# Kernel tuning notes

Hardware: AMD Instinct MI355X
Metric: run time of the kernel (lower is better)

The kernel has to match this reference:

```python
import jax, jax.numpy as jnp
import numpy as np
from jax import lax

WIN = 9
PAD = WIN // 2  # floor(9/2) = 4, 'same' spatial output


def _box_sum(x):
    # 3D sliding-window sum via conv with a ones kernel [1,1,9,9,9]
    k = jnp.ones((1, 1, WIN, WIN, WIN), x.dtype)
    return lax.conv_general_dilated(
        x, k,
        window_strides=(1, 1, 1),
        padding=[(PAD, PAD)] * 3,
        dimension_numbers=('NCDHW', 'OIDHW', 'NCDHW'),
    )


def setup_inputs() -> dict:
    key = jax.random.key(0)
    k1, k2 = jax.random.split(key)
    shape = (2, 1, 160, 160, 160)  # [B, C=1, D, H, W] 3D volumes
    return {
        'y_true': jax.random.normal(k1, shape, dtype=jnp.float32),
        'y_pred': jax.random.normal(k2, shape, dtype=jnp.float32),
    }


def reference(y_true, y_pred):
    win_size = float(WIN ** 3)  # 729
    I, J = y_true, y_pred
    I_sum = _box_sum(I)
    J_sum = _box_sum(J)
    I2_sum = _box_sum(I * I)
    J2_sum = _box_sum(J * J)
    IJ_sum = _box_sum(I * J)
    u_I = I_sum / win_size
    u_J = J_sum / win_size
    cross = IJ_sum - u_J * I_sum - u_I * J_sum + u_I * u_J * win_size
    I_var = I2_sum - 2.0 * u_I * I_sum + u_I * u_I * win_size
    J_var = J2_sum - 2.0 * u_J * J_sum + u_J * u_J * win_size
    cc = cross * cross / (I_var * J_var + 1e-5)
    return -jnp.mean(cc)
```

## Files before the change

kernel.cpp:

```cpp
#include <hip/hip_runtime.h>


#define NB   2
#define NDIM 160
#define TILE 32
#define RE   40
#define HS   42
#define DCHUNK 32
#define NDCHUNK (NDIM / DCHUNK)
#define NSLICE (DCHUNK + 8)
#define NBLK ((NDIM/TILE)*(NDIM/TILE)*NB*NDCHUNK)
#define NTHR 1024
#define SLICE_SZ (NDIM * NDIM)

__device__ __forceinline__ float both_halves_sum(float a) {
#if __has_builtin(__builtin_amdgcn_permlane32_swap)
    typedef int v2i __attribute__((ext_vector_type(2)));
    v2i r = __builtin_amdgcn_permlane32_swap(__float_as_int(a),
                                             __float_as_int(a), false, false);
    return __int_as_float(r[0]) + __int_as_float(r[1]);
#else
    return a + __shfl_xor(a, 32, 64);
#endif
}

__global__ __launch_bounds__(NTHR)
void ncc_main(const float* __restrict__ I, const float* __restrict__ J,
              double* __restrict__ out_acc, unsigned int* __restrict__ out_cnt,
              float* __restrict__ out) {
    const int t  = threadIdx.x;
    const int tx = t & 31;
    const int ty = t >> 5;
    const int half = ty & 1;
    const int w0 = blockIdx.x * TILE;
    const int h0 = blockIdx.y * TILE;
    const int b  = blockIdx.z / NDCHUNK;
    const int d0 = (blockIdx.z % NDCHUNK) * DCHUNK;

    const float* Ib = I + (size_t)b * NDIM * SLICE_SZ;
    const float* Jb = J + (size_t)b * NDIM * SLICE_SZ;

    __shared__ alignas(16) float sI[2][RE][HS];
    __shared__ alignas(16) float sJ[2][RE][HS];
    __shared__ float4 rs4[RE][TILE + 1];
    __shared__ float  rss[RE][TILE + 1];
    __shared__ double wsum[NTHR / 64];

    const int e1 = t + NTHR;
    const int r0 = t / RE,  c0 = t - r0 * RE;
    const int r1 = e1 / RE, c1 = e1 - r1 * RE;
    const int h_0 = h0 - 4 + r0, w_0 = w0 - 4 + c0;
    const int h_1 = h0 - 4 + r1, w_1 = w0 - 4 + c1;
    const bool has1 = (e1 < RE * RE);
    const bool in0 = ((unsigned)h_0 < NDIM) && ((unsigned)w_0 < NDIM);
    const bool in1 = has1 && ((unsigned)h_1 < NDIM) && ((unsigned)w_1 < NDIM);
    const int idx0 = h_0 * NDIM + w_0;
    const int idx1 = h_1 * NDIM + w_1;

    const int br  = t >> 4;
    const int bw0 = (t & 15) * 2;
    const int rb = (ty & ~1) + half * 5;
    const int re = (ty & ~1) + (half ? 0 : 9);

    float ring[9][5];
#pragma unroll
    for (int k = 0; k < 9; ++k)
#pragma unroll
        for (int c = 0; c < 5; ++c) ring[k][c] = 0.0f;

    float acc[5] = {0.f, 0.f, 0.f, 0.f, 0.f};
    double csum = 0.0;
    const float inv_win = 1.0f / 729.0f;
    int cur = 0;

    {
        const int dz0 = d0 - 4;
        if ((unsigned)dz0 < NDIM) {
            const float* Iz = Ib + (size_t)dz0 * SLICE_SZ;
            const float* Jz = Jb + (size_t)dz0 * SLICE_SZ;
            sI[0][r0][c0] = in0 ? Iz[idx0] : 0.f;
            sJ[0][r0][c0] = in0 ? Jz[idx0] : 0.f;
            if (has1) {
                sI[0][r1][c1] = in1 ? Iz[idx1] : 0.f;
                sJ[0][r1][c1] = in1 ? Jz[idx1] : 0.f;
            }
        }
        __syncthreads();
    }

    for (int o = 0; o < 5; ++o) {
#pragma unroll
        for (int j = 0; j < 9; ++j) {
            const int step = o * 9 + j;
            const int dz = d0 - 4 + step;
            float s[5] = {0.f, 0.f, 0.f, 0.f, 0.f};
            if (step < NSLICE) {
                const int dzn = dz + 1;
                const bool pf = (step + 1 < NSLICE) && ((unsigned)dzn < NDIM);
                float pvi0 = 0.f, pvj0 = 0.f, pvi1 = 0.f, pvj1 = 0.f;
                if (pf) {
                    const float* Iz = Ib + (size_t)dzn * SLICE_SZ;
                    const float* Jz = Jb + (size_t)dzn * SLICE_SZ;
                    if (in0) { pvi0 = Iz[idx0]; pvj0 = Jz[idx0]; }
                    if (in1) { pvi1 = Iz[idx1]; pvj1 = Jz[idx1]; }
                }
                if ((unsigned)dz < NDIM && t < 640) {
                    const float2* pI = (const float2*)(&sI[cur][br][bw0]);
                    const float2* pJ = (const float2*)(&sJ[cur][br][bw0]);
                    float2 iA = pI[0], iB = pI[1], iC = pI[2], iD = pI[3], iE = pI[4];
                    float2 jA = pJ[0], jB = pJ[1], jC = pJ[2], jD = pJ[3], jE = pJ[4];
                    float aI  = iA.x + iA.y + iB.x + iB.y + iC.x + iC.y
                              + iD.x + iD.y + iE.x;
                    float aJ  = jA.x + jA.y + jB.x + jB.y + jC.x + jC.y
                              + jD.x + jD.y + jE.x;
                    float aI2 = iA.x*iA.x + iA.y*iA.y + iB.x*iB.x + iB.y*iB.y
                              + iC.x*iC.x + iC.y*iC.y + iD.x*iD.x + iD.y*iD.y
                              + iE.x*iE.x;
                    float aJ2 = jA.x*jA.x + jA.y*jA.y + jB.x*jB.x + jB.y*jB.y
                              + jC.x*jC.x + jC.y*jC.y + jD.x*jD.x + jD.y*jD.y
                              + jE.x*jE.x;
                    float aIJ = iA.x*jA.x + iA.y*jA.y + iB.x*jB.x + iB.y*jB.y
                              + iC.x*jC.x + iC.y*jC.y + iD.x*jD.x + iD.y*jD.y
                              + iE.x*jE.x;
                    rs4[br][bw0] = make_float4(aI, aJ, aI2, aJ2);
                    rss[br][bw0] = aIJ;
                    aI  += iE.y - iA.x;
                    aJ  += jE.y - jA.x;
                    aI2 += iE.y*iE.y - iA.x*iA.x;
                    aJ2 += jE.y*jE.y - jA.x*jA.x;
                    aIJ += iE.y*jE.y - iA.x*jA.x;
                    rs4[br][bw0 + 1] = make_float4(aI, aJ, aI2, aJ2);
                    rss[br][bw0 + 1] = aIJ;
                }
                if (pf) {
                    const int nxt = cur ^ 1;
                    sI[nxt][r0][c0] = pvi0;
                    sJ[nxt][r0][c0] = pvj0;
                    if (has1) { sI[nxt][r1][c1] = pvi1; sJ[nxt][r1][c1] = pvj1; }
                }
                __syncthreads();
                if ((unsigned)dz < NDIM) {
                    float a0 = 0.f, a1 = 0.f, a2 = 0.f, a3 = 0.f, a4 = 0.f;
#pragma unroll
                    for (int k = 0; k < 5; ++k) {
                        float4 v = rs4[rb + k][tx];
                        a0 += v.x; a1 += v.y; a2 += v.z; a3 += v.w;
                        a4 += rss[rb + k][tx];
                    }
                    float4 ev = rs4[re][tx];
                    float  es = rss[re][tx];
                    s[0] = both_halves_sum(a0) - ev.x;
                    s[1] = both_halves_sum(a1) - ev.y;
                    s[2] = both_halves_sum(a2) - ev.z;
                    s[3] = both_halves_sum(a3) - ev.w;
                    s[4] = both_halves_sum(a4) - es;
                }
                __syncthreads();
                cur ^= 1;
            }
#pragma unroll
            for (int c = 0; c < 5; ++c) {
                acc[c] += s[c] - ring[j][c];
                ring[j][c] = s[c];
            }
            if (step >= 8 && step < 8 + DCHUNK) {
                float Is = acc[0], Js = acc[1];
                float I2 = acc[2], J2 = acc[3], IJ = acc[4];
                float cross = IJ - Is * Js * inv_win;
                float Ivar  = I2 - Is * Is * inv_win;
                float Jvar  = J2 - Js * Js * inv_win;
                float cc = cross * cross / (Ivar * Jvar + 1e-5f);
                csum += (double)cc;
            }
        }
    }

#pragma unroll
    for (int off = 32; off > 0; off >>= 1)
        csum += __shfl_down(csum, off, 64);
    if ((t & 63) == 0) wsum[t >> 6] = csum;
    __syncthreads();
    if (t == 0) {
        double total = 0.0;
#pragma unroll
        for (int wv = 0; wv < NTHR / 64; ++wv) total += wsum[wv];
        atomicAdd(out_acc, total);
        __threadfence();
        unsigned int old = atomicAdd(out_cnt, 1u);
        if (old == NBLK - 1) {
            double fin = atomicAdd(out_acc, 0.0);
            out[0] = (float)(-fin / 8192000.0);
        }
    }
}

extern "C" void kernel_launch(void* const* d_in, const int* in_sizes, int n_in,
                              void* d_out, int out_size, void* d_ws, size_t ws_size,
                              hipStream_t stream) {
    const float* I = (const float*)d_in[0];
    const float* J = (const float*)d_in[1];
    double* acc = (double*)d_ws;
    unsigned int* cnt = (unsigned int*)((char*)d_ws + 8);

    hipMemsetAsync(d_ws, 0, 16, stream);

    dim3 grid(NDIM / TILE, NDIM / TILE, NB * NDCHUNK);
    ncc_main<<<grid, NTHR, 0, stream>>>(I, J, acc, cnt, (float*)d_out);
}
```

Measured before the change: 140.2 us.

## Load halo slices as float4 and double-buffer row sums to drop a barrier

Slice staging now uses 128-bit float4 global loads. Each of 960 threads loads four contiguous floats of either I or J into a 48-wide padded row, replacing four scalar loads per thread. The row-sum buffers rs4/rss are double-buffered by slice parity, so the second __syncthreads per slice is removed. This halves the barriers per step and cuts load instruction count, at the cost of more shared memory. Correctness relies on the 4-aligned tile edges, where a float4 is either fully inside the volume or fully outside.

```diff
diff --git a/kernel.cpp b/kernel.cpp
--- a/kernel.cpp
+++ b/kernel.cpp
@@ -5,7 +5,7 @@
 #define NDIM 160
 #define TILE 32
 #define RE   40
-#define HS   42
+#define F4W  12
 #define DCHUNK 32
 #define NDCHUNK (NDIM / DCHUNK)
 #define NSLICE (DCHUNK + 8)
@@ -40,22 +40,20 @@
     const float* Ib = I + (size_t)b * NDIM * SLICE_SZ;
     const float* Jb = J + (size_t)b * NDIM * SLICE_SZ;
 
-    __shared__ alignas(16) float sI[2][RE][HS];
-    __shared__ alignas(16) float sJ[2][RE][HS];
-    __shared__ float4 rs4[RE][TILE + 1];
-    __shared__ float  rss[RE][TILE + 1];
+    __shared__ float4 sH[2][2][RE][F4W];
+    __shared__ float4 rs4[2][RE][TILE + 1];
+    __shared__ float  rss[2][RE][TILE + 1];
     __shared__ double wsum[NTHR / 64];
 
-    const int e1 = t + NTHR;
-    const int r0 = t / RE,  c0 = t - r0 * RE;
-    const int r1 = e1 / RE, c1 = e1 - r1 * RE;
-    const int h_0 = h0 - 4 + r0, w_0 = w0 - 4 + c0;
-    const int h_1 = h0 - 4 + r1, w_1 = w0 - 4 + c1;
-    const bool has1 = (e1 < RE * RE);
-    const bool in0 = ((unsigned)h_0 < NDIM) && ((unsigned)w_0 < NDIM);
-    const bool in1 = has1 && ((unsigned)h_1 < NDIM) && ((unsigned)w_1 < NDIM);
-    const int idx0 = h_0 * NDIM + w_0;
-    const int idx1 = h_1 * NDIM + w_1;
+    const int sa   = (t / 480) & 1;
+    const int item = t - (t / 480) * 480;
+    const int sr   = item / F4W;
+    const int sf   = item - sr * F4W;
+    const int sgr  = h0 - 4 + sr;
+    const int sgc  = w0 - 8 + 4 * sf;
+    const bool sval = (t < 960) && ((unsigned)sgr < NDIM) &&
+                      ((unsigned)sgc < NDIM) && (sgc + 3 < NDIM);
+    const int sgoff = sgr * NDIM + sgc;
 
     const int br  = t >> 4;
     const int bw0 = (t & 15) * 2;
@@ -71,19 +69,15 @@
     float acc[5] = {0.f, 0.f, 0.f, 0.f, 0.f};
     double csum = 0.0;
     const float inv_win = 1.0f / 729.0f;
-    int cur = 0;
+    int bi = 0;
 
     {
         const int dz0 = d0 - 4;
-        if ((unsigned)dz0 < NDIM) {
-            const float* Iz = Ib + (size_t)dz0 * SLICE_SZ;
-            const float* Jz = Jb + (size_t)dz0 * SLICE_SZ;
-            sI[0][r0][c0] = in0 ? Iz[idx0] : 0.f;
-            sJ[0][r0][c0] = in0 ? Jz[idx0] : 0.f;
-            if (has1) {
-                sI[0][r1][c1] = in1 ? Iz[idx1] : 0.f;
-                sJ[0][r1][c1] = in1 ? Jz[idx1] : 0.f;
-            }
+        if ((unsigned)dz0 < NDIM && t < 960) {
+            const float* base = (sa ? Jb : Ib) + (size_t)dz0 * SLICE_SZ;
+            float4 v = make_float4(0.f, 0.f, 0.f, 0.f);
+            if (sval) v = *reinterpret_cast<const float4*>(base + sgoff);
+            sH[0][sa][sr][sf] = v;
         }
         __syncthreads();
     }
@@ -97,16 +91,16 @@
             if (step < NSLICE) {
                 const int dzn = dz + 1;
                 const bool pf = (step + 1 < NSLICE) && ((unsigned)dzn < NDIM);
-                float pvi0 = 0.f, pvj0 = 0.f, pvi1 = 0.f, pvj1 = 0.f;
-                if (pf) {
-                    const float* Iz = Ib + (size_t)dzn * SLICE_SZ;
-                    const float* Jz = Jb + (size_t)dzn * SLICE_SZ;
-                    if (in0) { pvi0 = Iz[idx0]; pvj0 = Jz[idx0]; }
-                    if (in1) { pvi1 = Iz[idx1]; pvj1 = Jz[idx1]; }
+                float4 pv = make_float4(0.f, 0.f, 0.f, 0.f);
+                if (pf && sval) {
+                    const float* base = (sa ? Jb : Ib) + (size_t)dzn * SLICE_SZ;
+                    pv = *reinterpret_cast<const float4*>(base + sgoff);
                 }
                 if ((unsigned)dz < NDIM && t < 640) {
-                    const float2* pI = (const float2*)(&sI[cur][br][bw0]);
-                    const float2* pJ = (const float2*)(&sJ[cur][br][bw0]);
+                    const float* rowI = (const float*)sH[bi][0][br];
+                    const float* rowJ = (const float*)sH[bi][1][br];
+                    const float2* pI = (const float2*)(rowI + bw0 + 4);
+                    const float2* pJ = (const float2*)(rowJ + bw0 + 4);
                     float2 iA = pI[0], iB = pI[1], iC = pI[2], iD = pI[3], iE = pI[4];
                     float2 jA = pJ[0], jB = pJ[1], jC = pJ[2], jD = pJ[3], jE = pJ[4];
                     float aI  = iA.x + iA.y + iB.x + iB.y + iC.x + iC.y
@@ -122,41 +116,35 @@
                     float aIJ = iA.x*jA.x + iA.y*jA.y + iB.x*jB.x + iB.y*jB.y
                               + iC.x*jC.x + iC.y*jC.y + iD.x*jD.x + iD.y*jD.y
                               + iE.x*jE.x;
-                    rs4[br][bw0] = make_float4(aI, aJ, aI2, aJ2);
-                    rss[br][bw0] = aIJ;
+                    rs4[bi][br][bw0] = make_float4(aI, aJ, aI2, aJ2);
+                    rss[bi][br][bw0] = aIJ;
                     aI  += iE.y - iA.x;
                     aJ  += jE.y - jA.x;
                     aI2 += iE.y*iE.y - iA.x*iA.x;
                     aJ2 += jE.y*jE.y - jA.x*jA.x;
                     aIJ += iE.y*jE.y - iA.x*jA.x;
-                    rs4[br][bw0 + 1] = make_float4(aI, aJ, aI2, aJ2);
-                    rss[br][bw0 + 1] = aIJ;
+                    rs4[bi][br][bw0 + 1] = make_float4(aI, aJ, aI2, aJ2);
+                    rss[bi][br][bw0 + 1] = aIJ;
                 }
-                if (pf) {
-                    const int nxt = cur ^ 1;
-                    sI[nxt][r0][c0] = pvi0;
-                    sJ[nxt][r0][c0] = pvj0;
-                    if (has1) { sI[nxt][r1][c1] = pvi1; sJ[nxt][r1][c1] = pvj1; }
-                }
+                if (pf && t < 960) sH[bi ^ 1][sa][sr][sf] = pv;
                 __syncthreads();
                 if ((unsigned)dz < NDIM) {
                     float a0 = 0.f, a1 = 0.f, a2 = 0.f, a3 = 0.f, a4 = 0.f;
 #pragma unroll
                     for (int k = 0; k < 5; ++k) {
-                        float4 v = rs4[rb + k][tx];
+                        float4 v = rs4[bi][rb + k][tx];
                         a0 += v.x; a1 += v.y; a2 += v.z; a3 += v.w;
-                        a4 += rss[rb + k][tx];
+                        a4 += rss[bi][rb + k][tx];
                     }
-                    float4 ev = rs4[re][tx];
-                    float  es = rss[re][tx];
+                    float4 ev = rs4[bi][re][tx];
+                    float  es = rss[bi][re][tx];
                     s[0] = both_halves_sum(a0) - ev.x;
                     s[1] = both_halves_sum(a1) - ev.y;
                     s[2] = both_halves_sum(a2) - ev.z;
                     s[3] = both_halves_sum(a3) - ev.w;
                     s[4] = both_halves_sum(a4) - es;
                 }
-                __syncthreads();
-                cur ^= 1;
+                bi ^= 1;
             }
 #pragma unroll
             for (int c = 0; c < 5; ++c) {
```

New measurement: 140.3 us. About the same (+0.1%).
